# Performance work log

Hardware: AMD Instinct MI355X
Metric: run time of the kernel (lower is better)

The kernel has to match this reference:

```python
import jax, jax.numpy as jnp
import numpy as np

N_NODES = 100000
N_EDGES = 800000
VOCAB = 256      # node_dict_size
NODE_DIM = 256
HIDDEN = 256
N_MASK = 10000


def setup_inputs() -> dict:
    key = jax.random.key(0)
    ks = jax.random.split(key, 8)
    return {
        "x": jax.random.randint(ks[0], (N_NODES, 1), 0, VOCAB, dtype=jnp.int64 if jax.config.jax_enable_x64 else jnp.int32),
        "edge_index": jax.random.randint(ks[1], (2, N_EDGES), 0, N_NODES, dtype=jnp.int32),
        "mask_x_position": jax.random.randint(ks[2], (N_MASK,), 0, N_NODES, dtype=jnp.int32),
        "emb": jax.random.normal(ks[3], (VOCAB, NODE_DIM), dtype=jnp.float32) * (NODE_DIM ** -0.5),
        "W1": jax.random.normal(ks[4], (NODE_DIM, HIDDEN), dtype=jnp.float32) * (NODE_DIM ** -0.5),
        "b1": jnp.zeros((HIDDEN,), dtype=jnp.float32),
        "W2": jax.random.normal(ks[5], (HIDDEN, VOCAB), dtype=jnp.float32) * (HIDDEN ** -0.5),
        "b2": jnp.zeros((VOCAB,), dtype=jnp.float32),
    }


def _gcn_conv(h, W, b, src, dst, norm, n_nodes):
    # PyG GCNConv: out = scatter_add(norm * (h @ W)[src], dst) + b
    hw = h @ W                                      # [N, out]
    msgs = hw[src] * norm[:, None]                  # [E+N, out]
    out = jax.ops.segment_sum(msgs, dst, num_segments=n_nodes)
    return out + b


def _gcn_norm(edge_index, n_nodes):
    # add self-loops, compute sym-normalized edge weights (PyG gcn_norm)
    loops = jnp.arange(n_nodes, dtype=edge_index.dtype)
    src = jnp.concatenate([edge_index[0], loops])
    dst = jnp.concatenate([edge_index[1], loops])
    deg = jax.ops.segment_sum(jnp.ones_like(dst, dtype=jnp.float32), dst,
                              num_segments=n_nodes)  # in-degree incl. self-loop
    dinv = jnp.where(deg > 0, jax.lax.rsqrt(deg), 0.0)
    norm = dinv[src] * dinv[dst]                    # [E+N]
    return src, dst, norm


def reference(x, edge_index, mask_x_position, emb, W1, b1, W2, b2):
    n_nodes = x.shape[0]
    src, dst, norm = _gcn_norm(edge_index, n_nodes)
    h = emb[x[:, 0]]                                # Embedding + squeeze(1) -> [N, node_dim]
    # dropout p=0 / eval mode -> identity
    h = _gcn_conv(h, W1, b1, src, dst, norm, n_nodes)
    h = jax.nn.relu(h)
    h = _gcn_conv(h, W2, b2, src, dst, norm, n_nodes)  # [N, vocab]
    return jax.nn.log_softmax(h[mask_x_position], axis=1)
```

## Files before the change

kernel.cpp:

```cpp
#include <hip/hip_runtime.h>
#include <stdint.h>

#define NN 100000
#define NE 800000
#define ND 256
#define NM 10000
#define NMP 10048
#define NPB 128
#define NBK 782
#define BCAP 1280
#define TILE 1024
#define EBK ((NE + TILE - 1) / TILE)

typedef __attribute__((ext_vector_type(8))) short bf16x8;
typedef __attribute__((ext_vector_type(4))) float f32x4;

__device__ __forceinline__ float bf2f(unsigned short u) {
    return __uint_as_float(((unsigned)u) << 16);
}
__device__ __forceinline__ unsigned short f2bf(float f) {
    unsigned u = __float_as_uint(f);
    u += 0x7fffu + ((u >> 16) & 1u);
    return (unsigned short)(u >> 16);
}


__global__ void k_maskmap(const int* __restrict__ mpos, int* __restrict__ minfo,
                          unsigned char* __restrict__ mb, unsigned char* __restrict__ fb,
                          int* __restrict__ gcur, int* __restrict__ nctr) {
    int j = blockIdx.x * 256 + threadIdx.x;
    if (j < NM) {
        int p = mpos[j];
        minfo[p] = (j + 1) << 1;
        mb[p] = 1;
        fb[p] = 1;
    }
    if (j < NBK) gcur[j] = j * BCAP;
    if (j == 0) *nctr = 0;
}

__global__ __launch_bounds__(256) void k_bin(
    const int* __restrict__ src, const int* __restrict__ dst,
    const unsigned char* __restrict__ mb, unsigned char* __restrict__ fb,
    int* __restrict__ gcur, int* __restrict__ ebuf,
    const float* __restrict__ emb, const float* __restrict__ W1,
    const float* __restrict__ W2,
    unsigned short* __restrict__ M1, unsigned short* __restrict__ W2t) {
    __shared__ int lcnt[NBK];
    __shared__ int sd[TILE], ss[TILE];
    __shared__ float er[ND];
    int b = blockIdx.x, t = threadIdx.x;
    if (b >= EBK) {
        int bb = b - EBK;
        if (bb < ND) {
            er[t] = emb[bb * ND + t];
            __syncthreads();
            float acc = 0.f;
            for (int k = 0; k < ND; k++) acc += er[k] * W1[k * ND + t];
            M1[bb * ND + t] = f2bf(acc);
        } else {
            int n = bb - ND;
            W2t[n * ND + t] = f2bf(W2[t * ND + n]);
        }
        return;
    }
    for (int i = t; i < NBK; i += 256) lcnt[i] = 0;
    __syncthreads();
    int e0 = b * TILE;
#pragma unroll
    for (int k = 0; k < TILE / 256; k++) {
        int idx = t + k * 256;
        int e = e0 + idx;
        if (e < NE) {
            int d = dst[e], s = src[e];
            sd[idx] = d; ss[idx] = s;
            atomicAdd(&lcnt[d >> 7], 1);
            if (mb[d] == 1) fb[s] = 1;
        }
    }
    __syncthreads();
    for (int i = t; i < NBK; i += 256) {
        int c = lcnt[i];
        lcnt[i] = c ? atomicAdd(&gcur[i], c) : 0;
    }
    __syncthreads();
    int nv = min(NE - e0, TILE);
#pragma unroll
    for (int k = 0; k < TILE / 256; k++) {
        int idx = t + k * 256;
        if (idx < nv) {
            int d = sd[idx], s = ss[idx];
            int bk = d >> 7, j = d & 127;
            int pos = atomicAdd(&lcnt[bk], 1);
            if (pos < (bk + 1) * BCAP) ebuf[pos] = s | (j << 17);
        }
    }
}

__global__ void k_bhist(const int* __restrict__ gcur, const int* __restrict__ ebuf,
                        const int* __restrict__ x, const unsigned char* __restrict__ mb,
                        const unsigned char* __restrict__ fb,
                        int* __restrict__ carr, int4* __restrict__ xd4,
                        int* __restrict__ nlist, int* __restrict__ nctr,
                        int* __restrict__ part) {
    __shared__ int bins[NPB];
    __shared__ int rs[4];
    int b = blockIdx.x, t = threadIdx.x;
    int lane = t & 63, wv = t >> 6;
    if (t < NPB) bins[t] = 0;
    __syncthreads();
    int n = min(gcur[b] - b * BCAP, BCAP);
    int base = b * BCAP;
    for (int i = t; i < n; i += 256)
        atomicAdd(&bins[ebuf[base + i] >> 17], 1);
    __syncthreads();
    int node = b * NPB + t;
    int w = 0;
    if (t < NPB && node < NN) {
        int c = bins[t];
        carr[node] = c;
        float dv = rsqrtf((float)c + 1.0f);
        int cc = 0;
        if (fb[node] == 1) {
            cc = atomicAdd(nctr, 1);
            nlist[cc] = node;
        }
        xd4[node] = make_int4(x[node], __float_as_int(dv), cc, 0);
        w = c + ((mb[node] == 1) ? c : 0);
    }
#pragma unroll
    for (int o = 32; o >= 1; o >>= 1) w += __shfl_xor(w, o, 64);
    if (lane == 0) rs[wv] = w;
    __syncthreads();
    if (t == 0) part[b] = rs[0] + rs[1] + rs[2] + rs[3];
}

__global__ __launch_bounds__(256) void k_place(
    const int* __restrict__ gcur, const int* __restrict__ ebuf,
    const int* __restrict__ minfo, const unsigned char* __restrict__ fb,
    const int* __restrict__ carr, const int* __restrict__ part,
    const int4* __restrict__ xd4, int* __restrict__ off, int2* __restrict__ pairs) {
    __shared__ int sinfo[NPB], lc1[NPB], lc2[NPB];
    __shared__ int bred[4], wtot[2];
    int b = blockIdx.x, t = threadIdx.x;
    int lane = t & 63, wv = t >> 6;
    int pv = 0;
    for (int i = t; i < b; i += 256) pv += part[i];
#pragma unroll
    for (int o = 32; o >= 1; o >>= 1) pv += __shfl_xor(pv, o, 64);
    if (lane == 0) bred[wv] = pv;
    __syncthreads();
    int pbase = bred[0] + bred[1] + bred[2] + bred[3];
    int node = b * NPB + t;
    int c = 0, m = 0, f = 0;
    if (t < NPB && node < NN) {
        c = carr[node];
        int mv = minfo[node];
        if (mv > 0) m = mv;
        f = (fb[node] == 1) ? 1 : 0;
    }
    int wgt = (t < NPB) ? (c + (m ? c : 0)) : 0;
    int xx = wgt;
    for (int o = 1; o < 64; o <<= 1) { int y = __shfl_up(xx, o, 64); if (lane >= o) xx += y; }
    if (lane == 63 && wv < 2) wtot[wv] = xx;
    __syncthreads();
    if (t < NPB) {
        int excl = xx - wgt + ((wv == 1) ? wtot[0] : 0);
        int myoff = pbase + excl;
        if (node < NN) off[node] = myoff;
        sinfo[t] = m | f;
        lc1[t] = myoff;
        lc2[t] = myoff + c;
    }
    __syncthreads();
    int n = min(gcur[b] - b * BCAP, BCAP);
    int base = b * BCAP;
    for (int i = t; i < n; i += 256) {
        int w = ebuf[base + i];
        int j = w >> 17, s = w & 0x1FFFF;
        int ii = sinfo[j];
        if (ii == 0) continue;
        int4 xv = xd4[s];
        if (ii & 1) {
            int p = atomicAdd(&lc1[j], 1);
            pairs[p] = make_int2(xv.x, xv.y);
        }
        if (ii > 1) {
            int p = atomicAdd(&lc2[j], 1);
            pairs[p] = make_int2(xv.z, xv.y);
        }
    }
}

__global__ void k_expand(const int* __restrict__ nctr, const int* __restrict__ nlist,
                         const int4* __restrict__ xd4,
                         const int* __restrict__ off, const int* __restrict__ carr,
                         const int2* __restrict__ pairs,
                         const unsigned short* __restrict__ M1,
                         const float* __restrict__ b1,
                         unsigned short* __restrict__ h1c) {
    int lane = threadIdx.x & 63;
    int wave = (blockIdx.x * 256 + threadIdx.x) >> 6;
    if (wave >= *nctr) return;
    int i = nlist[wave];
    float4 b1v = ((const float4*)b1)[lane];
    int4 x0 = xd4[i];
    int v0 = x0.x;
    float w0 = __int_as_float(x0.y);
    ushort4 mm = *(const ushort4*)(M1 + (size_t)v0 * ND + lane * 4);
    float a0 = w0 * bf2f(mm.x), a1 = w0 * bf2f(mm.y);
    float a2 = w0 * bf2f(mm.z), a3 = w0 * bf2f(mm.w);
    int e = off[i], end = e + carr[i];
    for (; e + 4 <= end; e += 4) {
        int2 pA = pairs[e + 0];
        int2 pB = pairs[e + 1];
        int2 pC = pairs[e + 2];
        int2 pD = pairs[e + 3];
        ushort4 mA = *(const ushort4*)(M1 + (size_t)pA.x * ND + lane * 4);
        ushort4 mB = *(const ushort4*)(M1 + (size_t)pB.x * ND + lane * 4);
        ushort4 mC = *(const ushort4*)(M1 + (size_t)pC.x * ND + lane * 4);
        ushort4 mD = *(const ushort4*)(M1 + (size_t)pD.x * ND + lane * 4);
        float wA = __int_as_float(pA.y), wB = __int_as_float(pB.y);
        float wC = __int_as_float(pC.y), wD = __int_as_float(pD.y);
        a0 += wA * bf2f(mA.x) + wB * bf2f(mB.x) + wC * bf2f(mC.x) + wD * bf2f(mD.x);
        a1 += wA * bf2f(mA.y) + wB * bf2f(mB.y) + wC * bf2f(mC.y) + wD * bf2f(mD.y);
        a2 += wA * bf2f(mA.z) + wB * bf2f(mB.z) + wC * bf2f(mC.z) + wD * bf2f(mD.z);
        a3 += wA * bf2f(mA.w) + wB * bf2f(mB.w) + wC * bf2f(mC.w) + wD * bf2f(mD.w);
    }
    for (; e < end; e++) {
        int2 p = pairs[e];
        float w = __int_as_float(p.y);
        ushort4 m2 = *(const ushort4*)(M1 + (size_t)p.x * ND + lane * 4);
        a0 += w * bf2f(m2.x);
        a1 += w * bf2f(m2.y);
        a2 += w * bf2f(m2.z);
        a3 += w * bf2f(m2.w);
    }
    ushort4 o;
    o.x = f2bf(fmaxf(fmaf(w0, a0, b1v.x), 0.f));
    o.y = f2bf(fmaxf(fmaf(w0, a1, b1v.y), 0.f));
    o.z = f2bf(fmaxf(fmaf(w0, a2, b1v.z), 0.f));
    o.w = f2bf(fmaxf(fmaf(w0, a3, b1v.w), 0.f));
    ((ushort4*)(h1c + (size_t)wave * ND))[lane] = o;
}

__global__ void k_agg2(const int* __restrict__ mpos, const int* __restrict__ minfo,
                       const int4* __restrict__ xd4,
                       const int2* __restrict__ pairs, const int* __restrict__ off,
                       const int* __restrict__ carr,
                       const unsigned short* __restrict__ h1c,
                       unsigned short* __restrict__ agg2b) {
    int lane = threadIdx.x & 63;
    int wave = (blockIdx.x * 256 + threadIdx.x) >> 6;
    if (wave >= NM) return;
    int r = wave;
    int p = mpos[r];
    if ((minfo[p] >> 1) != r + 1) return;
    int4 xp = xd4[p];
    int cp = xp.z;
    float dv = __int_as_float(xp.y);
    ushort4 h0 = *(const ushort4*)(h1c + (size_t)cp * ND + lane * 4);
    float a0 = dv * bf2f(h0.x), a1 = dv * bf2f(h0.y);
    float a2 = dv * bf2f(h0.z), a3 = dv * bf2f(h0.w);
    int c2 = carr[p];
    int e = off[p] + c2, end = e + c2;
    for (; e + 4 <= end; e += 4) {
        int2 pA = pairs[e + 0];
        int2 pB = pairs[e + 1];
        int2 pC = pairs[e + 2];
        int2 pD = pairs[e + 3];
        ushort4 hA = *(const ushort4*)(h1c + (size_t)pA.x * ND + lane * 4);
        ushort4 hB = *(const ushort4*)(h1c + (size_t)pB.x * ND + lane * 4);
        ushort4 hC = *(const ushort4*)(h1c + (size_t)pC.x * ND + lane * 4);
        ushort4 hD = *(const ushort4*)(h1c + (size_t)pD.x * ND + lane * 4);
        float wA = __int_as_float(pA.y), wB = __int_as_float(pB.y);
        float wC = __int_as_float(pC.y), wD = __int_as_float(pD.y);
        a0 += wA * bf2f(hA.x) + wB * bf2f(hB.x) + wC * bf2f(hC.x) + wD * bf2f(hD.x);
        a1 += wA * bf2f(hA.y) + wB * bf2f(hB.y) + wC * bf2f(hC.y) + wD * bf2f(hD.y);
        a2 += wA * bf2f(hA.z) + wB * bf2f(hB.z) + wC * bf2f(hC.z) + wD * bf2f(hD.z);
        a3 += wA * bf2f(hA.w) + wB * bf2f(hB.w) + wC * bf2f(hC.w) + wD * bf2f(hD.w);
    }
    for (; e < end; e++) {
        int2 pp = pairs[e];
        float w = __int_as_float(pp.y);
        ushort4 hv = *(const ushort4*)(h1c + (size_t)pp.x * ND + lane * 4);
        a0 += w * bf2f(hv.x);
        a1 += w * bf2f(hv.y);
        a2 += w * bf2f(hv.z);
        a3 += w * bf2f(hv.w);
    }
    ushort4 o;
    o.x = f2bf(dv * a0);
    o.y = f2bf(dv * a1);
    o.z = f2bf(dv * a2);
    o.w = f2bf(dv * a3);
    ((ushort4*)(agg2b + (size_t)r * ND))[lane] = o;
}

__global__ __launch_bounds__(256) void k_out2(
    const int* __restrict__ mpos, const int* __restrict__ minfo,
    const unsigned short* __restrict__ agg2b, const unsigned short* __restrict__ W2t,
    const float* __restrict__ b2, float* __restrict__ out) {
    int lane = threadIdx.x & 63;
    int wv = threadIdx.x >> 6;
    int row0 = blockIdx.x * 64 + wv * 16;
    int qm = lane & 15, qk = lane >> 4;
    int row = row0 + qm;
    bf16x8 afr[8];
    if (row < NM) {
        int p = mpos[row];
        int rr = (minfo[p] >> 1) - 1;
        const unsigned short* arow = agg2b + (size_t)rr * ND + qk * 8;
#pragma unroll
        for (int kt = 0; kt < 8; kt++) afr[kt] = *(const bf16x8*)(arow + kt * 32);
    } else {
#pragma unroll
        for (int kt = 0; kt < 8; kt++) afr[kt] = (bf16x8){0, 0, 0, 0, 0, 0, 0, 0};
    }
    f32x4 acc[16];
#pragma unroll
    for (int t = 0; t < 16; t++) acc[t] = (f32x4){0.f, 0.f, 0.f, 0.f};
#pragma unroll
    for (int t = 0; t < 16; t++) {
        const unsigned short* brow = W2t + (size_t)(t * 16 + qm) * ND + qk * 8;
#pragma unroll
        for (int kt = 0; kt < 8; kt++) {
            bf16x8 bfr = *(const bf16x8*)(brow + kt * 32);
            acc[t] = __builtin_amdgcn_mfma_f32_16x16x32_bf16(afr[kt], bfr, acc[t], 0, 0, 0);
        }
    }
    float mx[4] = {-1e30f, -1e30f, -1e30f, -1e30f};
#pragma unroll
    for (int t = 0; t < 16; t++) {
        float cb = b2[qm + 16 * t];
#pragma unroll
        for (int r = 0; r < 4; r++) {
            float v = acc[t][r] + cb;
            acc[t][r] = v;
            mx[r] = fmaxf(mx[r], v);
        }
    }
#pragma unroll
    for (int r = 0; r < 4; r++)
        for (int o = 1; o < 16; o <<= 1) mx[r] = fmaxf(mx[r], __shfl_xor(mx[r], o, 64));
    float sm[4] = {0.f, 0.f, 0.f, 0.f};
#pragma unroll
    for (int t = 0; t < 16; t++)
#pragma unroll
        for (int r = 0; r < 4; r++) sm[r] += __expf(acc[t][r] - mx[r]);
#pragma unroll
    for (int r = 0; r < 4; r++)
        for (int o = 1; o < 16; o <<= 1) sm[r] += __shfl_xor(sm[r], o, 64);
#pragma unroll
    for (int r = 0; r < 4; r++) {
        int orow_i = row0 + qk * 4 + r;
        if (orow_i >= NM) continue;
        float lse = mx[r] + __logf(sm[r]);
        float* orow = out + (size_t)orow_i * ND + qm;
#pragma unroll
        for (int t = 0; t < 16; t++) orow[16 * t] = acc[t][r] - lse;
    }
}

extern "C" void kernel_launch(void* const* d_in, const int* in_sizes, int n_in,
                              void* d_out, int out_size, void* d_ws, size_t ws_size,
                              hipStream_t stream) {
    const int* x    = (const int*)d_in[0];
    const int* ei   = (const int*)d_in[1];
    const int* src  = ei;
    const int* dst  = ei + NE;
    const int* mpos = (const int*)d_in[2];
    const float* emb = (const float*)d_in[3];
    const float* W1  = (const float*)d_in[4];
    const float* b1  = (const float*)d_in[5];
    const float* W2  = (const float*)d_in[6];
    const float* b2  = (const float*)d_in[7];
    float* out = (float*)d_out;

    char* w = (char*)d_ws;
    size_t o = 0;
    int*   carr  = (int*)(w + o);  o += (size_t)(NN + 64) * 4;
    int*   off   = (int*)(w + o);  o += (size_t)(NN + 64) * 4;
    int*   minfo = (int*)(w + o);  o += (size_t)NN * 4;
    unsigned char* mb = (unsigned char*)(w + o); o += (size_t)(NN + 64);
    unsigned char* fb = (unsigned char*)(w + o); o += (size_t)(NN + 64);
    int4*  xd4   = (int4*)(w + o); o += (size_t)NN * 16;
    int*   nlist = (int*)(w + o);  o += (size_t)NN * 4;
    int*   nctr  = (int*)(w + o);  o += 64;
    int*   part  = (int*)(w + o);  o += 1024 * 4;
    int*   gcur  = (int*)(w + o);  o += (size_t)(NBK + 64) * 4;
    int*   ebuf  = (int*)(w + o);  o += (size_t)NBK * BCAP * 4;
    unsigned short* M1    = (unsigned short*)(w + o); o += (size_t)ND * ND * 2;
    unsigned short* W2t   = (unsigned short*)(w + o); o += (size_t)ND * ND * 2;
    unsigned short* agg2b = (unsigned short*)(w + o); o += (size_t)NM * ND * 2;
    int2*  pairs = (int2*)(w + o); o += (size_t)NE * 2 * 8;
    unsigned short* h1c  = (unsigned short*)(w + o); o += (size_t)NN * ND * 2;

    k_maskmap<<<(NM + 255) / 256, 256, 0, stream>>>(mpos, minfo, mb, fb, gcur, nctr);
    k_bin<<<EBK + 2 * ND, 256, 0, stream>>>(src, dst, mb, fb, gcur, ebuf,
                                            emb, W1, W2, M1, W2t);
    k_bhist<<<NBK, 256, 0, stream>>>(gcur, ebuf, x, mb, fb, carr, xd4, nlist, nctr, part);
    k_place<<<NBK, 256, 0, stream>>>(gcur, ebuf, minfo, fb, carr, part, xd4, off, pairs);
    k_expand<<<(NN + 3) / 4, 256, 0, stream>>>(nctr, nlist, xd4, off, carr, pairs, M1, b1, h1c);
    k_agg2<<<(NM + 3) / 4, 256, 0, stream>>>(mpos, minfo, xd4, pairs, off, carr, h1c, agg2b);
    k_out2<<<NMP / 64, 256, 0, stream>>>(mpos, minfo, agg2b, W2t, b2, out);
}
```

Measured before the change: 206.0 us.

## Fuse histogram and placement kernels, simplify binning, shrink pair storage

```diff
diff --git a/kernel.cpp b/kernel.cpp
--- a/kernel.cpp
+++ b/kernel.cpp
@@ -9,8 +9,7 @@
 #define NPB 128
 #define NBK 782
 #define BCAP 1280
-#define TILE 1024
-#define EBK ((NE + TILE - 1) / TILE)
+#define NEB ((NE + 255) / 256)
 
 typedef __attribute__((ext_vector_type(8))) short bf16x8;
 typedef __attribute__((ext_vector_type(4))) float f32x4;
@@ -35,8 +34,8 @@
         mb[p] = 1;
         fb[p] = 1;
     }
-    if (j < NBK) gcur[j] = j * BCAP;
-    if (j == 0) *nctr = 0;
+    if (j < NBK) gcur[j << 4] = j * BCAP;
+    if (j == 0) { nctr[0] = 0; nctr[1] = 0; }
 }
 
 __global__ __launch_bounds__(256) void k_bin(
@@ -46,12 +45,10 @@
     const float* __restrict__ emb, const float* __restrict__ W1,
     const float* __restrict__ W2,
     unsigned short* __restrict__ M1, unsigned short* __restrict__ W2t) {
-    __shared__ int lcnt[NBK];
-    __shared__ int sd[TILE], ss[TILE];
     __shared__ float er[ND];
     int b = blockIdx.x, t = threadIdx.x;
-    if (b >= EBK) {
-        int bb = b - EBK;
+    if (b >= NEB) {
+        int bb = b - NEB;
         if (bb < ND) {
             er[t] = emb[bb * ND + t];
             __syncthreads();
@@ -64,130 +61,92 @@
         }
         return;
     }
-    for (int i = t; i < NBK; i += 256) lcnt[i] = 0;
-    __syncthreads();
-    int e0 = b * TILE;
-#pragma unroll
-    for (int k = 0; k < TILE / 256; k++) {
-        int idx = t + k * 256;
-        int e = e0 + idx;
-        if (e < NE) {
-            int d = dst[e], s = src[e];
-            sd[idx] = d; ss[idx] = s;
-            atomicAdd(&lcnt[d >> 7], 1);
-            if (mb[d] == 1) fb[s] = 1;
-        }
-    }
-    __syncthreads();
-    for (int i = t; i < NBK; i += 256) {
-        int c = lcnt[i];
-        lcnt[i] = c ? atomicAdd(&gcur[i], c) : 0;
-    }
-    __syncthreads();
-    int nv = min(NE - e0, TILE);
-#pragma unroll
-    for (int k = 0; k < TILE / 256; k++) {
-        int idx = t + k * 256;
-        if (idx < nv) {
-            int d = sd[idx], s = ss[idx];
-            int bk = d >> 7, j = d & 127;
-            int pos = atomicAdd(&lcnt[bk], 1);
-            if (pos < (bk + 1) * BCAP) ebuf[pos] = s | (j << 17);
-        }
-    }
-}
-
-__global__ void k_bhist(const int* __restrict__ gcur, const int* __restrict__ ebuf,
-                        const int* __restrict__ x, const unsigned char* __restrict__ mb,
-                        const unsigned char* __restrict__ fb,
-                        int* __restrict__ carr, int4* __restrict__ xd4,
-                        int* __restrict__ nlist, int* __restrict__ nctr,
-                        int* __restrict__ part) {
+    int e = b * 256 + t;
+    if (e < NE) {
+        int d = dst[e], s = src[e];
+        int bk = d >> 7;
+        int pos = atomicAdd(&gcur[bk << 4], 1);
+        if (pos < (bk + 1) * BCAP) ebuf[pos] = s | ((d & 127) << 17);
+        if (mb[d] == 1) fb[s] = 1;
+    }
+}
+
+__global__ __launch_bounds__(256) void k_build(
+    const int* __restrict__ gcur, const int* __restrict__ ebuf,
+    const int* __restrict__ x, const unsigned char* __restrict__ fb,
+    const int* __restrict__ minfo,
+    int* __restrict__ carr, int4* __restrict__ xd4,
+    int* __restrict__ nlist, int* __restrict__ nctr,
+    int* __restrict__ off, int* __restrict__ pairs) {
+    __shared__ int sE[BCAP];
     __shared__ int bins[NPB];
-    __shared__ int rs[4];
+    __shared__ int lc1[NPB], lc2[NPB], sinfo[NPB];
+    __shared__ int wtot[2];
+    __shared__ int sbase;
     int b = blockIdx.x, t = threadIdx.x;
     int lane = t & 63, wv = t >> 6;
+    int base = b * BCAP;
+    int n = min(gcur[b << 4] - base, BCAP);
+    for (int i = t; i < n; i += 256) sE[i] = ebuf[base + i];
     if (t < NPB) bins[t] = 0;
     __syncthreads();
-    int n = min(gcur[b] - b * BCAP, BCAP);
-    int base = b * BCAP;
-    for (int i = t; i < n; i += 256)
-        atomicAdd(&bins[ebuf[base + i] >> 17], 1);
-    __syncthreads();
-    int node = b * NPB + t;
-    int w = 0;
-    if (t < NPB && node < NN) {
-        int c = bins[t];
-        carr[node] = c;
-        float dv = rsqrtf((float)c + 1.0f);
-        int cc = 0;
-        if (fb[node] == 1) {
-            cc = atomicAdd(nctr, 1);
-            nlist[cc] = node;
-        }
-        xd4[node] = make_int4(x[node], __float_as_int(dv), cc, 0);
-        w = c + ((mb[node] == 1) ? c : 0);
-    }
-#pragma unroll
-    for (int o = 32; o >= 1; o >>= 1) w += __shfl_xor(w, o, 64);
-    if (lane == 0) rs[wv] = w;
-    __syncthreads();
-    if (t == 0) part[b] = rs[0] + rs[1] + rs[2] + rs[3];
-}
-
-__global__ __launch_bounds__(256) void k_place(
-    const int* __restrict__ gcur, const int* __restrict__ ebuf,
-    const int* __restrict__ minfo, const unsigned char* __restrict__ fb,
-    const int* __restrict__ carr, const int* __restrict__ part,
-    const int4* __restrict__ xd4, int* __restrict__ off, int2* __restrict__ pairs) {
-    __shared__ int sinfo[NPB], lc1[NPB], lc2[NPB];
-    __shared__ int bred[4], wtot[2];
-    int b = blockIdx.x, t = threadIdx.x;
-    int lane = t & 63, wv = t >> 6;
-    int pv = 0;
-    for (int i = t; i < b; i += 256) pv += part[i];
-#pragma unroll
-    for (int o = 32; o >= 1; o >>= 1) pv += __shfl_xor(pv, o, 64);
-    if (lane == 0) bred[wv] = pv;
-    __syncthreads();
-    int pbase = bred[0] + bred[1] + bred[2] + bred[3];
+    for (int i = t; i < n; i += 256) atomicAdd(&bins[sE[i] >> 17], 1);
+    __syncthreads();
     int node = b * NPB + t;
     int c = 0, m = 0, f = 0;
     if (t < NPB && node < NN) {
-        c = carr[node];
+        c = bins[t];
+        if (fb[node] == 1) f = 1;
         int mv = minfo[node];
         if (mv > 0) m = mv;
-        f = (fb[node] == 1) ? 1 : 0;
-    }
-    int wgt = (t < NPB) ? (c + (m ? c : 0)) : 0;
+    }
+    int cc = 0;
+    {
+        unsigned long long bal = __ballot(f);
+        if (bal) {
+            int ldr = (int)(__ffsll((long long)bal) - 1);
+            int bs = 0;
+            if (lane == ldr) bs = atomicAdd(&nctr[0], __popcll(bal));
+            bs = __shfl(bs, ldr, 64);
+            if (f) {
+                cc = bs + __popcll(bal & ((1ull << lane) - 1ull));
+                nlist[cc] = node;
+            }
+        }
+    }
+    if (t < NPB && node < NN) {
+        carr[node] = c;
+        float dv = rsqrtf((float)c + 1.0f);
+        xd4[node] = make_int4(x[node], __float_as_int(dv), cc, 0);
+    }
+    int wgt = (t < NPB) ? ((f ? c : 0) + (m ? c : 0)) : 0;
     int xx = wgt;
     for (int o = 1; o < 64; o <<= 1) { int y = __shfl_up(xx, o, 64); if (lane >= o) xx += y; }
     if (lane == 63 && wv < 2) wtot[wv] = xx;
     __syncthreads();
+    if (t == 0) sbase = atomicAdd(&nctr[1], wtot[0] + wtot[1]);
+    __syncthreads();
     if (t < NPB) {
         int excl = xx - wgt + ((wv == 1) ? wtot[0] : 0);
-        int myoff = pbase + excl;
+        int myoff = sbase + excl;
         if (node < NN) off[node] = myoff;
         sinfo[t] = m | f;
         lc1[t] = myoff;
         lc2[t] = myoff + c;
     }
     __syncthreads();
-    int n = min(gcur[b] - b * BCAP, BCAP);
-    int base = b * BCAP;
     for (int i = t; i < n; i += 256) {
-        int w = ebuf[base + i];
+        int w = sE[i];
         int j = w >> 17, s = w & 0x1FFFF;
         int ii = sinfo[j];
         if (ii == 0) continue;
-        int4 xv = xd4[s];
         if (ii & 1) {
             int p = atomicAdd(&lc1[j], 1);
-            pairs[p] = make_int2(xv.x, xv.y);
+            pairs[p] = s;
         }
         if (ii > 1) {
             int p = atomicAdd(&lc2[j], 1);
-            pairs[p] = make_int2(xv.z, xv.y);
+            pairs[p] = s;
         }
     }
 }
@@ -195,13 +154,13 @@
 __global__ void k_expand(const int* __restrict__ nctr, const int* __restrict__ nlist,
                          const int4* __restrict__ xd4,
                          const int* __restrict__ off, const int* __restrict__ carr,
-                         const int2* __restrict__ pairs,
+                         const int* __restrict__ pairs,
                          const unsigned short* __restrict__ M1,
                          const float* __restrict__ b1,
                          unsigned short* __restrict__ h1c) {
     int lane = threadIdx.x & 63;
     int wave = (blockIdx.x * 256 + threadIdx.x) >> 6;
-    if (wave >= *nctr) return;
+    if (wave >= nctr[0]) return;
     int i = nlist[wave];
     float4 b1v = ((const float4*)b1)[lane];
     int4 x0 = xd4[i];
@@ -212,25 +171,23 @@
     float a2 = w0 * bf2f(mm.z), a3 = w0 * bf2f(mm.w);
     int e = off[i], end = e + carr[i];
     for (; e + 4 <= end; e += 4) {
-        int2 pA = pairs[e + 0];
-        int2 pB = pairs[e + 1];
-        int2 pC = pairs[e + 2];
-        int2 pD = pairs[e + 3];
-        ushort4 mA = *(const ushort4*)(M1 + (size_t)pA.x * ND + lane * 4);
-        ushort4 mB = *(const ushort4*)(M1 + (size_t)pB.x * ND + lane * 4);
-        ushort4 mC = *(const ushort4*)(M1 + (size_t)pC.x * ND + lane * 4);
-        ushort4 mD = *(const ushort4*)(M1 + (size_t)pD.x * ND + lane * 4);
-        float wA = __int_as_float(pA.y), wB = __int_as_float(pB.y);
-        float wC = __int_as_float(pC.y), wD = __int_as_float(pD.y);
+        int sA = pairs[e + 0], sB = pairs[e + 1], sC = pairs[e + 2], sD = pairs[e + 3];
+        int4 xA = xd4[sA], xB = xd4[sB], xC = xd4[sC], xD = xd4[sD];
+        ushort4 mA = *(const ushort4*)(M1 + (size_t)xA.x * ND + lane * 4);
+        ushort4 mB = *(const ushort4*)(M1 + (size_t)xB.x * ND + lane * 4);
+        ushort4 mC = *(const ushort4*)(M1 + (size_t)xC.x * ND + lane * 4);
+        ushort4 mD = *(const ushort4*)(M1 + (size_t)xD.x * ND + lane * 4);
+        float wA = __int_as_float(xA.y), wB = __int_as_float(xB.y);
+        float wC = __int_as_float(xC.y), wD = __int_as_float(xD.y);
         a0 += wA * bf2f(mA.x) + wB * bf2f(mB.x) + wC * bf2f(mC.x) + wD * bf2f(mD.x);
         a1 += wA * bf2f(mA.y) + wB * bf2f(mB.y) + wC * bf2f(mC.y) + wD * bf2f(mD.y);
         a2 += wA * bf2f(mA.z) + wB * bf2f(mB.z) + wC * bf2f(mC.z) + wD * bf2f(mD.z);
         a3 += wA * bf2f(mA.w) + wB * bf2f(mB.w) + wC * bf2f(mC.w) + wD * bf2f(mD.w);
     }
     for (; e < end; e++) {
-        int2 p = pairs[e];
-        float w = __int_as_float(p.y);
-        ushort4 m2 = *(const ushort4*)(M1 + (size_t)p.x * ND + lane * 4);
+        int4 xv = xd4[pairs[e]];
+        float w = __int_as_float(xv.y);
+        ushort4 m2 = *(const ushort4*)(M1 + (size_t)xv.x * ND + lane * 4);
         a0 += w * bf2f(m2.x);
         a1 += w * bf2f(m2.y);
         a2 += w * bf2f(m2.z);
@@ -246,7 +203,7 @@
 
 __global__ void k_agg2(const int* __restrict__ mpos, const int* __restrict__ minfo,
                        const int4* __restrict__ xd4,
-                       const int2* __restrict__ pairs, const int* __restrict__ off,
+                       const int* __restrict__ pairs, const int* __restrict__ off,
                        const int* __restrict__ carr,
                        const unsigned short* __restrict__ h1c,
                        unsigned short* __restrict__ agg2b) {
@@ -265,25 +222,25 @@
     int c2 = carr[p];
     int e = off[p] + c2, end = e + c2;
     for (; e + 4 <= end; e += 4) {
-        int2 pA = pairs[e + 0];
-        int2 pB = pairs[e + 1];
-        int2 pC = pairs[e + 2];
-        int2 pD = pairs[e + 3];
-        ushort4 hA = *(const ushort4*)(h1c + (size_t)pA.x * ND + lane * 4);
-        ushort4 hB = *(const ushort4*)(h1c + (size_t)pB.x * ND + lane * 4);
-        ushort4 hC = *(const ushort4*)(h1c + (size_t)pC.x * ND + lane * 4);
-        ushort4 hD = *(const ushort4*)(h1c + (size_t)pD.x * ND + lane * 4);
-        float wA = __int_as_float(pA.y), wB = __int_as_float(pB.y);
-        float wC = __int_as_float(pC.y), wD = __int_as_float(pD.y);
+        int4 xA = xd4[pairs[e + 0]];
+        int4 xB = xd4[pairs[e + 1]];
+        int4 xC = xd4[pairs[e + 2]];
+        int4 xD = xd4[pairs[e + 3]];
+        ushort4 hA = *(const ushort4*)(h1c + (size_t)xA.z * ND + lane * 4);
+        ushort4 hB = *(const ushort4*)(h1c + (size_t)xB.z * ND + lane * 4);
+        ushort4 hC = *(const ushort4*)(h1c + (size_t)xC.z * ND + lane * 4);
+        ushort4 hD = *(const ushort4*)(h1c + (size_t)xD.z * ND + lane * 4);
+        float wA = __int_as_float(xA.y), wB = __int_as_float(xB.y);
+        float wC = __int_as_float(xC.y), wD = __int_as_float(xD.y);
         a0 += wA * bf2f(hA.x) + wB * bf2f(hB.x) + wC * bf2f(hC.x) + wD * bf2f(hD.x);
         a1 += wA * bf2f(hA.y) + wB * bf2f(hB.y) + wC * bf2f(hC.y) + wD * bf2f(hD.y);
         a2 += wA * bf2f(hA.z) + wB * bf2f(hB.z) + wC * bf2f(hC.z) + wD * bf2f(hD.z);
         a3 += wA * bf2f(hA.w) + wB * bf2f(hB.w) + wC * bf2f(hC.w) + wD * bf2f(hD.w);
     }
     for (; e < end; e++) {
-        int2 pp = pairs[e];
-        float w = __int_as_float(pp.y);
-        ushort4 hv = *(const ushort4*)(h1c + (size_t)pp.x * ND + lane * 4);
+        int4 xv = xd4[pairs[e]];
+        float w = __int_as_float(xv.y);
+        ushort4 hv = *(const ushort4*)(h1c + (size_t)xv.z * ND + lane * 4);
         a0 += w * bf2f(hv.x);
         a1 += w * bf2f(hv.y);
         a2 += w * bf2f(hv.z);
@@ -386,21 +343,20 @@
     unsigned char* fb = (unsigned char*)(w + o); o += (size_t)(NN + 64);
     int4*  xd4   = (int4*)(w + o); o += (size_t)NN * 16;
     int*   nlist = (int*)(w + o);  o += (size_t)NN * 4;
-    int*   nctr  = (int*)(w + o);  o += 64;
-    int*   part  = (int*)(w + o);  o += 1024 * 4;
-    int*   gcur  = (int*)(w + o);  o += (size_t)(NBK + 64) * 4;
+    int*   nctr  = (int*)(w + o);  o += 128;
+    int*   gcur  = (int*)(w + o);  o += (size_t)(NBK * 16 + 64) * 4;
     int*   ebuf  = (int*)(w + o);  o += (size_t)NBK * BCAP * 4;
     unsigned short* M1    = (unsigned short*)(w + o); o += (size_t)ND * ND * 2;
     unsigned short* W2t   = (unsigned short*)(w + o); o += (size_t)ND * ND * 2;
     unsigned short* agg2b = (unsigned short*)(w + o); o += (size_t)NM * ND * 2;
-    int2*  pairs = (int2*)(w + o); o += (size_t)NE * 2 * 8;
+    int*   pairs = (int*)(w + o);  o += (size_t)NE * 2 * 4;
     unsigned short* h1c  = (unsigned short*)(w + o); o += (size_t)NN * ND * 2;
 
     k_maskmap<<<(NM + 255) / 256, 256, 0, stream>>>(mpos, minfo, mb, fb, gcur, nctr);
-    k_bin<<<EBK + 2 * ND, 256, 0, stream>>>(src, dst, mb, fb, gcur, ebuf,
+    k_bin<<<NEB + 2 * ND, 256, 0, stream>>>(src, dst, mb, fb, gcur, ebuf,
                                             emb, W1, W2, M1, W2t);
-    k_bhist<<<NBK, 256, 0, stream>>>(gcur, ebuf, x, mb, fb, carr, xd4, nlist, nctr, part);
-    k_place<<<NBK, 256, 0, stream>>>(gcur, ebuf, minfo, fb, carr, part, xd4, off, pairs);
+    k_build<<<NBK, 256, 0, stream>>>(gcur, ebuf, x, fb, minfo, carr, xd4,
+                                     nlist, nctr, off, pairs);
     k_expand<<<(NN + 3) / 4, 256, 0, stream>>>(nctr, nlist, xd4, off, carr, pairs, M1, b1, h1c);
     k_agg2<<<(NM + 3) / 4, 256, 0, stream>>>(mpos, minfo, xd4, pairs, off, carr, h1c, agg2b);
     k_out2<<<NMP / 64, 256, 0, stream>>>(mpos, minfo, agg2b, W2t, b2, out);
```

After: 236.4 us. 1.15x slower.

## Stage M1 table in LDS and use compact per-node records in expand kernel

Applied to the files above, without the earlier changes.

```diff
diff --git a/kernel.cpp b/kernel.cpp
--- a/kernel.cpp
+++ b/kernel.cpp
@@ -139,7 +139,8 @@
     const int* __restrict__ gcur, const int* __restrict__ ebuf,
     const int* __restrict__ minfo, const unsigned char* __restrict__ fb,
     const int* __restrict__ carr, const int* __restrict__ part,
-    const int4* __restrict__ xd4, int* __restrict__ off, int2* __restrict__ pairs) {
+    const int4* __restrict__ xd4, int* __restrict__ off, int2* __restrict__ pairs,
+    int4* __restrict__ nrec) {
     __shared__ int sinfo[NPB], lc1[NPB], lc2[NPB];
     __shared__ int bred[4], wtot[2];
     int b = blockIdx.x, t = threadIdx.x;
@@ -167,7 +168,13 @@
     if (t < NPB) {
         int excl = xx - wgt + ((wv == 1) ? wtot[0] : 0);
         int myoff = pbase + excl;
-        if (node < NN) off[node] = myoff;
+        if (node < NN) {
+            off[node] = myoff;
+            if (f) {
+                int4 xv = xd4[node];
+                nrec[xv.z] = make_int4(xv.x, xv.y, myoff, c);
+            }
+        }
         sinfo[t] = m | f;
         lc1[t] = myoff;
         lc2[t] = myoff + c;
@@ -192,56 +199,63 @@
     }
 }
 
-__global__ void k_expand(const int* __restrict__ nctr, const int* __restrict__ nlist,
-                         const int4* __restrict__ xd4,
-                         const int* __restrict__ off, const int* __restrict__ carr,
-                         const int2* __restrict__ pairs,
-                         const unsigned short* __restrict__ M1,
-                         const float* __restrict__ b1,
-                         unsigned short* __restrict__ h1c) {
-    int lane = threadIdx.x & 63;
-    int wave = (blockIdx.x * 256 + threadIdx.x) >> 6;
-    if (wave >= *nctr) return;
-    int i = nlist[wave];
+__global__ __launch_bounds__(1024) void k_expand(
+    const int* __restrict__ nctr, const int4* __restrict__ nrec,
+    const int2* __restrict__ pairs,
+    const unsigned short* __restrict__ M1,
+    const float* __restrict__ b1,
+    unsigned short* __restrict__ h1c) {
+    __shared__ unsigned short sm1[ND * ND];
+    int t = threadIdx.x;
+    {
+        const uint4* g = (const uint4*)M1;
+        uint4* s = (uint4*)sm1;
+        for (int i = t; i < (ND * ND) / 8; i += 1024) s[i] = g[i];
+    }
+    __syncthreads();
+    int lane = t & 63;
     float4 b1v = ((const float4*)b1)[lane];
-    int4 x0 = xd4[i];
-    int v0 = x0.x;
-    float w0 = __int_as_float(x0.y);
-    ushort4 mm = *(const ushort4*)(M1 + (size_t)v0 * ND + lane * 4);
-    float a0 = w0 * bf2f(mm.x), a1 = w0 * bf2f(mm.y);
-    float a2 = w0 * bf2f(mm.z), a3 = w0 * bf2f(mm.w);
-    int e = off[i], end = e + carr[i];
-    for (; e + 4 <= end; e += 4) {
-        int2 pA = pairs[e + 0];
-        int2 pB = pairs[e + 1];
-        int2 pC = pairs[e + 2];
-        int2 pD = pairs[e + 3];
-        ushort4 mA = *(const ushort4*)(M1 + (size_t)pA.x * ND + lane * 4);
-        ushort4 mB = *(const ushort4*)(M1 + (size_t)pB.x * ND + lane * 4);
-        ushort4 mC = *(const ushort4*)(M1 + (size_t)pC.x * ND + lane * 4);
-        ushort4 mD = *(const ushort4*)(M1 + (size_t)pD.x * ND + lane * 4);
-        float wA = __int_as_float(pA.y), wB = __int_as_float(pB.y);
-        float wC = __int_as_float(pC.y), wD = __int_as_float(pD.y);
-        a0 += wA * bf2f(mA.x) + wB * bf2f(mB.x) + wC * bf2f(mC.x) + wD * bf2f(mD.x);
-        a1 += wA * bf2f(mA.y) + wB * bf2f(mB.y) + wC * bf2f(mC.y) + wD * bf2f(mD.y);
-        a2 += wA * bf2f(mA.z) + wB * bf2f(mB.z) + wC * bf2f(mC.z) + wD * bf2f(mD.z);
-        a3 += wA * bf2f(mA.w) + wB * bf2f(mB.w) + wC * bf2f(mC.w) + wD * bf2f(mD.w);
-    }
-    for (; e < end; e++) {
-        int2 p = pairs[e];
-        float w = __int_as_float(p.y);
-        ushort4 m2 = *(const ushort4*)(M1 + (size_t)p.x * ND + lane * 4);
-        a0 += w * bf2f(m2.x);
-        a1 += w * bf2f(m2.y);
-        a2 += w * bf2f(m2.z);
-        a3 += w * bf2f(m2.w);
-    }
-    ushort4 o;
-    o.x = f2bf(fmaxf(fmaf(w0, a0, b1v.x), 0.f));
-    o.y = f2bf(fmaxf(fmaf(w0, a1, b1v.y), 0.f));
-    o.z = f2bf(fmaxf(fmaf(w0, a2, b1v.z), 0.f));
-    o.w = f2bf(fmaxf(fmaf(w0, a3, b1v.w), 0.f));
-    ((ushort4*)(h1c + (size_t)wave * ND))[lane] = o;
+    int nw = nctr[0];
+    for (int idx = (blockIdx.x * 1024 + t) >> 6; idx < nw; idx += 4096) {
+        int4 rec = nrec[idx];
+        int v0 = rec.x;
+        float w0 = __int_as_float(rec.y);
+        ushort4 mm = *(const ushort4*)(sm1 + v0 * ND + lane * 4);
+        float a0 = w0 * bf2f(mm.x), a1 = w0 * bf2f(mm.y);
+        float a2 = w0 * bf2f(mm.z), a3 = w0 * bf2f(mm.w);
+        int e = rec.z, end = e + rec.w;
+        for (; e + 4 <= end; e += 4) {
+            int2 pA = pairs[e + 0];
+            int2 pB = pairs[e + 1];
+            int2 pC = pairs[e + 2];
+            int2 pD = pairs[e + 3];
+            ushort4 mA = *(const ushort4*)(sm1 + pA.x * ND + lane * 4);
+            ushort4 mB = *(const ushort4*)(sm1 + pB.x * ND + lane * 4);
+            ushort4 mC = *(const ushort4*)(sm1 + pC.x * ND + lane * 4);
+            ushort4 mD = *(const ushort4*)(sm1 + pD.x * ND + lane * 4);
+            float wA = __int_as_float(pA.y), wB = __int_as_float(pB.y);
+            float wC = __int_as_float(pC.y), wD = __int_as_float(pD.y);
+            a0 += wA * bf2f(mA.x) + wB * bf2f(mB.x) + wC * bf2f(mC.x) + wD * bf2f(mD.x);
+            a1 += wA * bf2f(mA.y) + wB * bf2f(mB.y) + wC * bf2f(mC.y) + wD * bf2f(mD.y);
+            a2 += wA * bf2f(mA.z) + wB * bf2f(mB.z) + wC * bf2f(mC.z) + wD * bf2f(mD.z);
+            a3 += wA * bf2f(mA.w) + wB * bf2f(mB.w) + wC * bf2f(mC.w) + wD * bf2f(mD.w);
+        }
+        for (; e < end; e++) {
+            int2 p = pairs[e];
+            float w = __int_as_float(p.y);
+            ushort4 m2 = *(const ushort4*)(sm1 + p.x * ND + lane * 4);
+            a0 += w * bf2f(m2.x);
+            a1 += w * bf2f(m2.y);
+            a2 += w * bf2f(m2.z);
+            a3 += w * bf2f(m2.w);
+        }
+        ushort4 o;
+        o.x = f2bf(fmaxf(fmaf(w0, a0, b1v.x), 0.f));
+        o.y = f2bf(fmaxf(fmaf(w0, a1, b1v.y), 0.f));
+        o.z = f2bf(fmaxf(fmaf(w0, a2, b1v.z), 0.f));
+        o.w = f2bf(fmaxf(fmaf(w0, a3, b1v.w), 0.f));
+        ((ushort4*)(h1c + (size_t)idx * ND))[lane] = o;
+    }
 }
 
 __global__ void k_agg2(const int* __restrict__ mpos, const int* __restrict__ minfo,
@@ -379,29 +393,32 @@
 
     char* w = (char*)d_ws;
     size_t o = 0;
-    int*   carr  = (int*)(w + o);  o += (size_t)(NN + 64) * 4;
-    int*   off   = (int*)(w + o);  o += (size_t)(NN + 64) * 4;
-    int*   minfo = (int*)(w + o);  o += (size_t)NN * 4;
-    unsigned char* mb = (unsigned char*)(w + o); o += (size_t)(NN + 64);
-    unsigned char* fb = (unsigned char*)(w + o); o += (size_t)(NN + 64);
-    int4*  xd4   = (int4*)(w + o); o += (size_t)NN * 16;
-    int*   nlist = (int*)(w + o);  o += (size_t)NN * 4;
-    int*   nctr  = (int*)(w + o);  o += 64;
-    int*   part  = (int*)(w + o);  o += 1024 * 4;
-    int*   gcur  = (int*)(w + o);  o += (size_t)(NBK + 64) * 4;
-    int*   ebuf  = (int*)(w + o);  o += (size_t)NBK * BCAP * 4;
-    unsigned short* M1    = (unsigned short*)(w + o); o += (size_t)ND * ND * 2;
-    unsigned short* W2t   = (unsigned short*)(w + o); o += (size_t)ND * ND * 2;
-    unsigned short* agg2b = (unsigned short*)(w + o); o += (size_t)NM * ND * 2;
-    int2*  pairs = (int2*)(w + o); o += (size_t)NE * 2 * 8;
-    unsigned short* h1c  = (unsigned short*)(w + o); o += (size_t)NN * ND * 2;
+#define ALLOC(nbytes) ({ void* _p = (void*)(w + o); o = (o + (size_t)(nbytes) + 63) & ~(size_t)63; _p; })
+    int*   carr  = (int*)ALLOC((size_t)(NN + 64) * 4);
+    int*   off   = (int*)ALLOC((size_t)(NN + 64) * 4);
+    int*   minfo = (int*)ALLOC((size_t)NN * 4);
+    unsigned char* mb = (unsigned char*)ALLOC(NN + 64);
+    unsigned char* fb = (unsigned char*)ALLOC(NN + 64);
+    int4*  xd4   = (int4*)ALLOC((size_t)NN * 16);
+    int*   nlist = (int*)ALLOC((size_t)NN * 4);
+    int*   nctr  = (int*)ALLOC(64);
+    int*   part  = (int*)ALLOC(1024 * 4);
+    int*   gcur  = (int*)ALLOC((size_t)(NBK + 64) * 4);
+    int*   ebuf  = (int*)ALLOC((size_t)NBK * BCAP * 4);
+    unsigned short* M1    = (unsigned short*)ALLOC((size_t)ND * ND * 2);
+    unsigned short* W2t   = (unsigned short*)ALLOC((size_t)ND * ND * 2);
+    unsigned short* agg2b = (unsigned short*)ALLOC((size_t)NM * ND * 2);
+    int2*  pairs = (int2*)ALLOC((size_t)NE * 2 * 8);
+    int4*  nrec  = (int4*)ALLOC((size_t)NN * 16);
+    unsigned short* h1c  = (unsigned short*)ALLOC((size_t)NN * ND * 2);
+#undef ALLOC
 
     k_maskmap<<<(NM + 255) / 256, 256, 0, stream>>>(mpos, minfo, mb, fb, gcur, nctr);
     k_bin<<<EBK + 2 * ND, 256, 0, stream>>>(src, dst, mb, fb, gcur, ebuf,
                                             emb, W1, W2, M1, W2t);
     k_bhist<<<NBK, 256, 0, stream>>>(gcur, ebuf, x, mb, fb, carr, xd4, nlist, nctr, part);
-    k_place<<<NBK, 256, 0, stream>>>(gcur, ebuf, minfo, fb, carr, part, xd4, off, pairs);
-    k_expand<<<(NN + 3) / 4, 256, 0, stream>>>(nctr, nlist, xd4, off, carr, pairs, M1, b1, h1c);
+    k_place<<<NBK, 256, 0, stream>>>(gcur, ebuf, minfo, fb, carr, part, xd4, off, pairs, nrec);
+    k_expand<<<256, 1024, 0, stream>>>(nctr, nrec, pairs, M1, b1, h1c);
     k_agg2<<<(NM + 3) / 4, 256, 0, stream>>>(mpos, minfo, xd4, pairs, off, carr, h1c, agg2b);
     k_out2<<<NMP / 64, 256, 0, stream>>>(mpos, minfo, agg2b, W2t, b2, out);
 }
```

Result: faster. 201.6 us (-2.2%).
